# Kernel optimization log

Hardware: AMD Instinct MI355X
Metric: run time of the kernel (lower is better)

## Reference

```python
import jax, jax.numpy as jnp
import numpy as np

B, N, FH, H, FO = 8, 1024, 128, 8, 64
FIN = 2 * FH  # f_hid * 2
NEG = -1e9
SLOPE = 0.2  # leaky_relu negative slope (GAT default)


def setup_inputs() -> dict:
    key = jax.random.key(0)
    ks = jax.random.split(key, 10)
    x = jax.random.normal(ks[0], (B, FIN), jnp.float32)
    A = jax.random.randint(ks[1], (B, N, N), 0, 2, jnp.int32)  # 0/1 dense adjacency
    mask_zero = jnp.ones((B, N, 1), jnp.float32)  # node validity mask
    p_atten = jax.random.uniform(ks[2], (B, N), jnp.float32)  # unused in forward body
    e_atten = jax.random.uniform(ks[3], (B, N, FIN), jnp.float32)
    Npost = jax.random.normal(ks[4], (N, FIN), jnp.float32) * np.float32(1.0 / np.sqrt(FIN))  # kaiming-ish
    w = jax.random.normal(ks[5], (H, FIN, FO), jnp.float32) * np.float32(1.0 / np.sqrt(FIN))
    a_src = jax.random.normal(ks[6], (H, FO), jnp.float32) * np.float32(0.1)
    a_dst = jax.random.normal(ks[7], (H, FO), jnp.float32) * np.float32(0.1)
    bias = jnp.zeros((FO,), jnp.float32)
    return {"x": x, "A": A, "mask_zero": mask_zero, "p_atten": p_atten,
            "e_atten": e_atten, "Npost": Npost, "w": w, "a_src": a_src,
            "a_dst": a_dst, "bias": bias}


def reference(x, A, mask_zero, p_atten, e_atten, Npost, w, a_src, a_dst, bias):
    # broadcast-mul feature gating: x [B,FIN] repeated over N posts, gated by Npost*e_atten
    recx = x[:, None, :] * (Npost[None, :, :] * e_atten)          # [B,N,FIN]
    # BatchGAT (DeepInf-style multi-head graph attention, dropout disabled / eval mode)
    h = jnp.einsum('bnf,hfo->bhno', recx, w)                      # [B,H,N,FO]
    s = jnp.einsum('bhno,ho->bhn', h, a_src)                      # src attention term
    d = jnp.einsum('bhno,ho->bhn', h, a_dst)                      # dst attention term
    logits = jax.nn.leaky_relu(s[:, :, :, None] + d[:, :, None, :], SLOPE)  # [B,H,N,N]
    adj = (A > 0)[:, None, :, :]                                  # [B,1,N,N]
    logits = jnp.where(adj, logits, NEG)
    attn = jax.nn.softmax(logits, axis=-1)                        # masked row softmax
    out = jnp.einsum('bhnm,bhmo->bhno', attn, h) + bias           # aggregate neighbors
    out = out.mean(axis=1)                                        # average heads -> [B,N,FO]
    return out * mask_zero                                        # zero padded nodes
```

## Files before the change

kernel.cpp:

```cpp
#include <hip/hip_runtime.h>

typedef __attribute__((ext_vector_type(8))) short          bf16x8;
typedef __attribute__((ext_vector_type(8))) unsigned short u16x8;
typedef __attribute__((ext_vector_type(4))) unsigned short u16x4;
typedef __attribute__((ext_vector_type(4))) float          f32x4;
typedef __attribute__((ext_vector_type(4))) unsigned int   u32x4;

union U8 { u16x8 u; bf16x8 b; u32x4 w; };
union U4 { u16x4 u; unsigned w[2]; };

__device__ __forceinline__ unsigned short f2bf(float f){
  unsigned u = __float_as_uint(f);
  return (unsigned short)((u + 0x7fffu + ((u >> 16) & 1u)) >> 16);
}
__device__ __forceinline__ unsigned pack_bf16(float lo, float hi){
  unsigned a = __float_as_uint(hi) + 0x8000u;
  unsigned b = __float_as_uint(lo) + 0x8000u;
  return __builtin_amdgcn_perm(a, b, 0x07060302u);
}

#define NN  1024
#define FIN 256
#define NH  8
#define FO  64

__global__ __launch_bounds__(256) void stage0(
    const float* __restrict__ w, const int* __restrict__ A,
    const float* __restrict__ bias, const float* __restrict__ mz,
    unsigned short* __restrict__ wfrag, unsigned long long* __restrict__ Abits,
    float* __restrict__ out)
{
  const int tid = blockIdx.x * 256 + threadIdx.x;
  if (tid < 16384){
    const int lane = tid & 63, ss = (tid >> 6) & 3, kc = (tid >> 8) & 7, h = tid >> 11;
    const int o = 16 * ss + (lane & 15);
    const int f = kc * 32 + (lane >> 4) * 8;
    u16x8 r;
    #pragma unroll
    for (int j = 0; j < 8; j++) r[j] = f2bf(w[(h * FIN + f + j) * FO + o]);
    *(u16x8*)(wfrag + tid * 8) = r;
  }
  #pragma unroll
  for (int k = 0; k < 2; k++){
    const int i = tid + k * 262144;
    out[i] = bias[i & 63] * mz[i >> 6];
  }
  for (int i = tid; i < 8388608; i += 262144){
    unsigned long long m = __ballot(A[i] > 0);
    if ((threadIdx.x & 63) == 0) Abits[i >> 6] = m;
  }
}

__global__ __launch_bounds__(512, 4) void stageA(
    const float* __restrict__ x, const float* __restrict__ e_at,
    const float* __restrict__ Np, const unsigned short* __restrict__ wfrag,
    const float* __restrict__ a_src, const float* __restrict__ a_dst,
    unsigned short* __restrict__ hT,
    float* __restrict__ exps, float* __restrict__ exps2,
    float* __restrict__ expd, float* __restrict__ expd2)
{
  __shared__ unsigned short rex[16 * 264];
  const int t = threadIdx.x;
  const int n0 = blockIdx.x * 16, b = blockIdx.y;

  {
    const int row = t >> 5, f0 = (t & 31) * 8;
    const int nrow = n0 + row;
    const float* ep = e_at + (b * NN + nrow) * FIN + f0;
    const float* qp = Np + nrow * FIN + f0;
    const float* xp = x + b * FIN + f0;
    f32x4 e0 = *(const f32x4*)ep, e1 = *(const f32x4*)(ep + 4);
    f32x4 q0 = *(const f32x4*)qp, q1 = *(const f32x4*)(qp + 4);
    f32x4 x0 = *(const f32x4*)xp, x1 = *(const f32x4*)(xp + 4);
    u16x8 r;
    #pragma unroll
    for (int j = 0; j < 4; j++){
      r[j]     = f2bf(e0[j] * q0[j] * x0[j]);
      r[j + 4] = f2bf(e1[j] * q1[j] * x1[j]);
    }
    *(u16x8*)(rex + row * 264 + f0) = r;
  }
  __syncthreads();

  const int h = t >> 6, lane = t & 63, quad = lane >> 4, l15 = lane & 15;
  const unsigned short* wf = wfrag + h * 16384 + lane * 8;

  f32x4 acc[4] = {};
  #pragma unroll
  for (int kc = 0; kc < 8; kc++){
    U8 a0, bf[4];
    a0.u = *(const u16x8*)(rex + l15 * 264 + kc * 32 + quad * 8);
    #pragma unroll
    for (int ss = 0; ss < 4; ss++) bf[ss].u = *(const u16x8*)(wf + (kc * 4 + ss) * 512);
    #pragma unroll
    for (int ss = 0; ss < 4; ss++)
      acc[ss] = __builtin_amdgcn_mfma_f32_16x16x32_bf16(a0.b, bf[ss].b, acc[ss], 0, 0, 0);
  }

  {
    const int mtile = blockIdx.x >> 1, moff = (blockIdx.x & 1) * 16;
    unsigned short* pan = hT + (size_t)(((b * NH + h) * 32 + mtile) * 64) * 32;
    #pragma unroll
    for (int ss = 0; ss < 4; ss++){
      U4 v;
      v.w[0] = pack_bf16(acc[ss][0], acc[ss][1]);
      v.w[1] = pack_bf16(acc[ss][2], acc[ss][3]);
      *(u16x4*)(pan + (16 * ss + l15) * 32 + moff + quad * 4) = v.u;
    }
  }

  float as4[4], ad4[4];
  #pragma unroll
  for (int ss = 0; ss < 4; ss++){
    as4[ss] = a_src[h * FO + 16 * ss + l15];
    ad4[ss] = a_dst[h * FO + 16 * ss + l15];
  }
  #pragma unroll
  for (int i = 0; i < 4; i++){
    float ps = 0.f, pd = 0.f;
    #pragma unroll
    for (int ss = 0; ss < 4; ss++){ ps += acc[ss][i] * as4[ss]; pd += acc[ss][i] * ad4[ss]; }
    #pragma unroll
    for (int off = 1; off < 16; off <<= 1){
      ps += __shfl_xor(ps, off);
      pd += __shfl_xor(pd, off);
    }
    if (l15 == 0){
      const int idx = (b * NH + h) * NN + n0 + quad * 4 + i;
      exps [idx] = __expf(ps);
      exps2[idx] = __expf(0.2f * ps);
      expd [idx] = __expf(pd);
      expd2[idx] = __expf(0.2f * pd);
    }
  }
}

__global__ __launch_bounds__(512, 8) void stageB(
    const unsigned* __restrict__ Aw,
    const unsigned short* __restrict__ hT,
    const float* __restrict__ exps, const float* __restrict__ exps2,
    const float* __restrict__ expd, const float* __restrict__ expd2,
    const float* __restrict__ mz, float* __restrict__ out)
{
  __shared__ float ed_l[2 * NN];
  __shared__ float e2_l[2 * NN];
  __shared__ unsigned mask_l[32 * 33];
  __shared__ float l_l[4 * 16];
  const int t = threadIdx.x;
  const int n0 = blockIdx.x * 32, hq = blockIdx.y, b = blockIdx.z;
  const int w = t >> 6, lane = t & 63, quad = lane >> 4, l15 = lane & 15;
  const int hl = w & 1, rg = (w >> 1) & 1, mh = w >> 2;
  const int h = hq * 2 + hl;

  if (t < 64) l_l[t] = 0.f;
  {
    const float* s1 = expd  + (b * NH + hq * 2) * NN;
    const float* s2 = expd2 + (b * NH + hq * 2) * NN;
    *(f32x4*)(ed_l + t * 4) = *(const f32x4*)(s1 + t * 4);
    *(f32x4*)(e2_l + t * 4) = *(const f32x4*)(s2 + t * 4);
  }
  #pragma unroll
  for (int k = 0; k < 2; k++){
    const int i = t + k * 512;
    mask_l[(i >> 5) * 33 + (i & 31)] = Aw[(b * NN + n0 + (i >> 5)) * 32 + (i & 31)];
  }
  __syncthreads();

  const int hb = (b * NH + h) * NN;
  const float Es  = exps [hb + n0 + rg * 16 + l15];
  const float Es2 = exps2[hb + n0 + rg * 16 + l15];
  const unsigned short* pb = hT + (size_t)(b * NH + h) * 65536 + l15 * 32 + quad * 8;
  const float* edh = ed_l + hl * NN + quad * 8;
  const float* e2h = e2_l + hl * NN + quad * 8;
  const unsigned* maskp = mask_l + (rg * 16 + l15) * 33;
  const int c0 = mh * 16;

  U8 pan[4];
  #pragma unroll
  for (int ss = 0; ss < 4; ss++)
    pan[ss].u = *(const u16x8*)(pb + (size_t)c0 * 2048 + ss * 512);

  f32x4 acc[4] = {};
  float lp = 0.f;

  for (int cc = 0; cc < 16; cc++){
    const int c = c0 + cc;
    const unsigned am = maskp[c] >> (quad * 8);
    float pv[8];
    #pragma unroll
    for (int g2 = 0; g2 < 2; g2++){
      f32x4 dv = *(const f32x4*)(edh + c * 32 + g2 * 4);
      f32x4 gv = *(const f32x4*)(e2h + c * 32 + g2 * 4);
      #pragma unroll
      for (int j = 0; j < 4; j++){
        float e = fmaxf(Es * dv[j], Es2 * gv[j]);
        pv[g2 * 4 + j] = (am & (1u << (g2 * 4 + j))) ? e : 0.f;
      }
    }
    lp += ((pv[0] + pv[1]) + (pv[2] + pv[3])) + ((pv[4] + pv[5]) + (pv[6] + pv[7]));
    U8 p;
    #pragma unroll
    for (int r = 0; r < 4; r++) p.w[r] = pack_bf16(pv[2 * r], pv[2 * r + 1]);
    #pragma unroll
    for (int ss = 0; ss < 4; ss++)
      acc[ss] = __builtin_amdgcn_mfma_f32_16x16x32_bf16(p.b, pan[ss].b, acc[ss], 0, 0, 0);
    if (cc + 1 < 16){
      #pragma unroll
      for (int ss = 0; ss < 4; ss++)
        pan[ss].u = *(const u16x8*)(pb + (size_t)(c + 1) * 2048 + ss * 512);
    }
  }

  lp += __shfl_xor(lp, 16);
  lp += __shfl_xor(lp, 32);
  if (lane < 16) atomicAdd(&l_l[(w & 3) * 16 + lane], lp);
  __syncthreads();

  const float* mzp = mz + b * NN + n0 + rg * 16;
  #pragma unroll
  for (int i = 0; i < 4; i++){
    const int row = quad * 4 + i;
    const float invm = (0.125f / l_l[(w & 3) * 16 + row]) * mzp[row];
    float* op = out + (size_t)(b * NN + n0 + rg * 16 + row) * FO + l15;
    #pragma unroll
    for (int ss = 0; ss < 4; ss++)
      atomicAdd(op + ss * 16, acc[ss][i] * invm);
  }
}

extern "C" void kernel_launch(void* const* d_in, const int* in_sizes, int n_in,
                              void* d_out, int out_size, void* d_ws, size_t ws_size,
                              hipStream_t stream)
{
  (void)in_sizes; (void)n_in; (void)out_size; (void)ws_size;
  const float* x    = (const float*)d_in[0];
  const int*   A    = (const int*)d_in[1];
  const float* mz   = (const float*)d_in[2];
  const float* e_at = (const float*)d_in[4];
  const float* Np   = (const float*)d_in[5];
  const float* w    = (const float*)d_in[6];
  const float* asrc = (const float*)d_in[7];
  const float* adst = (const float*)d_in[8];
  const float* bias = (const float*)d_in[9];
  float* out = (float*)d_out;

  char* ws = (char*)d_ws;
  unsigned short* wfrag = (unsigned short*)ws;
  unsigned short* hT    = (unsigned short*)(ws + 262144);
  float* exps  = (float*)(ws + 8650752);
  float* exps2 = (float*)(ws + 8912896);
  float* expd  = (float*)(ws + 9175040);
  float* expd2 = (float*)(ws + 9437184);
  unsigned long long* Abits = (unsigned long long*)(ws + 9699328);

  stage0<<<dim3(1024), dim3(256), 0, stream>>>(w, A, bias, mz, wfrag, Abits, out);
  stageA<<<dim3(64, 8), dim3(512), 0, stream>>>(x, e_at, Np, wfrag, asrc, adst,
                                                hT, exps, exps2, expd, expd2);
  stageB<<<dim3(32, 4, 8), dim3(512), 0, stream>>>((const unsigned*)Abits, hT,
                                                   exps, exps2, expd, expd2,
                                                   mz, out);
}
```

Measured before the change: 170.4 us.

## Split attention into row-sum pass and column-tiled aggregation with prescaled weights

Replaces the single stageB kernel with two kernels. phaseL computes each row's masked softmax denominator up front and folds 1/sum, the head-averaging factor and the node mask into per-row scale factors. phaseM then tiles over neighbor columns, stages the matching h panel in shared memory once per block and reuses it across all 1024 rows. Each tile's contribution goes to the output through atomics, with no per-block row-sum reduction. This trades an extra launch and computing the exponentials twice for much less re-reading of hT and more independent MFMA work, at the cost of more global atomics.

```diff
diff --git a/kernel.cpp b/kernel.cpp
--- a/kernel.cpp
+++ b/kernel.cpp
@@ -4,6 +4,7 @@
 typedef __attribute__((ext_vector_type(8))) unsigned short u16x8;
 typedef __attribute__((ext_vector_type(4))) unsigned short u16x4;
 typedef __attribute__((ext_vector_type(4))) float          f32x4;
+typedef __attribute__((ext_vector_type(4))) int            i32x4;
 typedef __attribute__((ext_vector_type(4))) unsigned int   u32x4;
 
 union U8 { u16x8 u; bf16x8 b; u32x4 w; };
@@ -135,96 +136,135 @@
   }
 }
 
-__global__ __launch_bounds__(512, 8) void stageB(
+__global__ __launch_bounds__(256, 4) void phaseL(
+    const unsigned* __restrict__ Aw,
+    const float* __restrict__ exps, const float* __restrict__ exps2,
+    const float* __restrict__ expd, const float* __restrict__ expd2,
+    const float* __restrict__ mz, float2* __restrict__ esc)
+{
+  __shared__ float ed[1024], e2[1024];
+  const int t = threadIdx.x;
+  const int h = blockIdx.y, b = blockIdx.z, bh = b * NH + h;
+  *(f32x4*)(ed + t * 4) = *(const f32x4*)(expd  + bh * NN + t * 4);
+  *(f32x4*)(e2 + t * 4) = *(const f32x4*)(expd2 + bh * NN + t * 4);
+  __syncthreads();
+
+  const int row = blockIdx.x * 64 + (t >> 2), q = t & 3;
+  const float Es = exps[bh * NN + row], Es2 = exps2[bh * NN + row];
+  const unsigned* mw = Aw + (b * NN + row) * 32 + q * 8;
+  i32x4 w0 = *(const i32x4*)mw, w1 = *(const i32x4*)(mw + 4);
+
+  float sum = 0.f;
+  #pragma unroll
+  for (int k = 0; k < 8; k++){
+    const unsigned wd = (unsigned)((k < 4) ? w0[k] : w1[k - 4]);
+    const int base = q * 256 + k * 32;
+    #pragma unroll
+    for (int g = 0; g < 8; g++){
+      f32x4 dv = *(const f32x4*)(ed + base + g * 4);
+      f32x4 gv = *(const f32x4*)(e2 + base + g * 4);
+      #pragma unroll
+      for (int j = 0; j < 4; j++){
+        const float e = fmaxf(Es * dv[j], Es2 * gv[j]);
+        sum += (wd & (1u << (g * 4 + j))) ? e : 0.f;
+      }
+    }
+  }
+  sum += __shfl_xor(sum, 1);
+  sum += __shfl_xor(sum, 2);
+  if (q == 0){
+    const float s = 0.125f * mz[b * NN + row] / sum;
+    float2 r; r.x = Es * s; r.y = Es2 * s;
+    esc[bh * NN + row] = r;
+  }
+}
+
+__global__ __launch_bounds__(512, 4) void phaseM(
     const unsigned* __restrict__ Aw,
     const unsigned short* __restrict__ hT,
-    const float* __restrict__ exps, const float* __restrict__ exps2,
     const float* __restrict__ expd, const float* __restrict__ expd2,
-    const float* __restrict__ mz, float* __restrict__ out)
-{
-  __shared__ float ed_l[2 * NN];
-  __shared__ float e2_l[2 * NN];
-  __shared__ unsigned mask_l[32 * 33];
-  __shared__ float l_l[4 * 16];
+    const float2* __restrict__ esc, float* __restrict__ out)
+{
+  __shared__ unsigned short pan[4 * 64 * 40];
+  __shared__ float ed[128], e2[128];
   const int t = threadIdx.x;
-  const int n0 = blockIdx.x * 32, hq = blockIdx.y, b = blockIdx.z;
-  const int w = t >> 6, lane = t & 63, quad = lane >> 4, l15 = lane & 15;
-  const int hl = w & 1, rg = (w >> 1) & 1, mh = w >> 2;
-  const int h = hq * 2 + hl;
-
-  if (t < 64) l_l[t] = 0.f;
+  const int mo = blockIdx.x, h = blockIdx.y, b = blockIdx.z, bh = b * NH + h;
+
   {
-    const float* s1 = expd  + (b * NH + hq * 2) * NN;
-    const float* s2 = expd2 + (b * NH + hq * 2) * NN;
-    *(f32x4*)(ed_l + t * 4) = *(const f32x4*)(s1 + t * 4);
-    *(f32x4*)(e2_l + t * 4) = *(const f32x4*)(s2 + t * 4);
-  }
-  #pragma unroll
-  for (int k = 0; k < 2; k++){
-    const int i = t + k * 512;
-    mask_l[(i >> 5) * 33 + (i & 31)] = Aw[(b * NN + n0 + (i >> 5)) * 32 + (i & 31)];
-  }
+    const unsigned short* src = hT + (size_t)(bh * 32 + mo * 4) * 2048 + t * 16;
+    u16x8 v0 = *(const u16x8*)src;
+    u16x8 v1 = *(const u16x8*)(src + 8);
+    const int g = t * 16, c = g >> 11, rem = g & 2047, o = rem >> 5, m0 = rem & 31;
+    unsigned short* dst = pan + (c * 64 + o) * 40 + m0;
+    *(u16x8*)dst = v0;
+    *(u16x8*)(dst + 8) = v1;
+  }
+  if (t < 32)      *(f32x4*)(ed + t * 4)        = *(const f32x4*)(expd  + bh * NN + mo * 128 + t * 4);
+  else if (t < 64) *(f32x4*)(e2 + (t - 32) * 4) = *(const f32x4*)(expd2 + bh * NN + mo * 128 + (t - 32) * 4);
   __syncthreads();
 
-  const int hb = (b * NH + h) * NN;
-  const float Es  = exps [hb + n0 + rg * 16 + l15];
-  const float Es2 = exps2[hb + n0 + rg * 16 + l15];
-  const unsigned short* pb = hT + (size_t)(b * NH + h) * 65536 + l15 * 32 + quad * 8;
-  const float* edh = ed_l + hl * NN + quad * 8;
-  const float* e2h = e2_l + hl * NN + quad * 8;
-  const unsigned* maskp = mask_l + (rg * 16 + l15) * 33;
-  const int c0 = mh * 16;
-
-  U8 pan[4];
-  #pragma unroll
-  for (int ss = 0; ss < 4; ss++)
-    pan[ss].u = *(const u16x8*)(pb + (size_t)c0 * 2048 + ss * 512);
-
-  f32x4 acc[4] = {};
-  float lp = 0.f;
-
-  for (int cc = 0; cc < 16; cc++){
-    const int c = c0 + cc;
-    const unsigned am = maskp[c] >> (quad * 8);
-    float pv[8];
-    #pragma unroll
-    for (int g2 = 0; g2 < 2; g2++){
-      f32x4 dv = *(const f32x4*)(edh + c * 32 + g2 * 4);
-      f32x4 gv = *(const f32x4*)(e2h + c * 32 + g2 * 4);
+  const int wv = t >> 6, lane = t & 63, quad = lane >> 4, l15 = lane & 15;
+  const unsigned* Ab = Aw + (size_t)(b * NN) * 32 + mo * 4;
+  const float2* ep = esc + bh * NN;
+
+  i32x4 pm0 = *(const i32x4*)(Ab + (size_t)(wv * 32 + l15) * 32);
+  i32x4 pm1 = *(const i32x4*)(Ab + (size_t)(wv * 32 + 16 + l15) * 32);
+  float2 pe0 = ep[wv * 32 + l15];
+  float2 pe1 = ep[wv * 32 + 16 + l15];
+
+  for (int nt = wv; nt < 32; nt += 8){
+    const i32x4 cm0 = pm0, cm1 = pm1;
+    const float2 ce0 = pe0, ce1 = pe1;
+    if (nt + 8 < 32){
+      pm0 = *(const i32x4*)(Ab + (size_t)((nt + 8) * 32 + l15) * 32);
+      pm1 = *(const i32x4*)(Ab + (size_t)((nt + 8) * 32 + 16 + l15) * 32);
+      pe0 = ep[(nt + 8) * 32 + l15];
+      pe1 = ep[(nt + 8) * 32 + 16 + l15];
+    }
+    f32x4 acc[2][4] = {};
+    #pragma unroll
+    for (int c = 0; c < 4; c++){
+      f32x4 dv0 = *(const f32x4*)(ed + c * 32 + quad * 8);
+      f32x4 dv1 = *(const f32x4*)(ed + c * 32 + quad * 8 + 4);
+      f32x4 gv0 = *(const f32x4*)(e2 + c * 32 + quad * 8);
+      f32x4 gv1 = *(const f32x4*)(e2 + c * 32 + quad * 8 + 4);
+      const unsigned a0 = ((unsigned)cm0[c]) >> (quad * 8);
+      const unsigned a1 = ((unsigned)cm1[c]) >> (quad * 8);
+      U8 p0, p1;
       #pragma unroll
-      for (int j = 0; j < 4; j++){
-        float e = fmaxf(Es * dv[j], Es2 * gv[j]);
-        pv[g2 * 4 + j] = (am & (1u << (g2 * 4 + j))) ? e : 0.f;
+      for (int r = 0; r < 4; r++){
+        const int j0 = 2 * r, j1 = 2 * r + 1;
+        const float d0 = (j0 < 4) ? dv0[j0] : dv1[j0 - 4];
+        const float g0 = (j0 < 4) ? gv0[j0] : gv1[j0 - 4];
+        const float d1 = (j1 < 4) ? dv0[j1] : dv1[j1 - 4];
+        const float g1 = (j1 < 4) ? gv0[j1] : gv1[j1 - 4];
+        float e00 = fmaxf(ce0.x * d0, ce0.y * g0);
+        float e01 = fmaxf(ce0.x * d1, ce0.y * g1);
+        float e10 = fmaxf(ce1.x * d0, ce1.y * g0);
+        float e11 = fmaxf(ce1.x * d1, ce1.y * g1);
+        e00 = (a0 & (1u << j0)) ? e00 : 0.f;
+        e01 = (a0 & (1u << j1)) ? e01 : 0.f;
+        e10 = (a1 & (1u << j0)) ? e10 : 0.f;
+        e11 = (a1 & (1u << j1)) ? e11 : 0.f;
+        p0.w[r] = pack_bf16(e00, e01);
+        p1.w[r] = pack_bf16(e10, e11);
       }
-    }
-    lp += ((pv[0] + pv[1]) + (pv[2] + pv[3])) + ((pv[4] + pv[5]) + (pv[6] + pv[7]));
-    U8 p;
-    #pragma unroll
-    for (int r = 0; r < 4; r++) p.w[r] = pack_bf16(pv[2 * r], pv[2 * r + 1]);
-    #pragma unroll
-    for (int ss = 0; ss < 4; ss++)
-      acc[ss] = __builtin_amdgcn_mfma_f32_16x16x32_bf16(p.b, pan[ss].b, acc[ss], 0, 0, 0);
-    if (cc + 1 < 16){
+      #pragma unroll
+      for (int ss = 0; ss < 4; ss++){
+        U8 pf;
+        pf.u = *(const u16x8*)(pan + (c * 64 + 16 * ss + l15) * 40 + quad * 8);
+        acc[0][ss] = __builtin_amdgcn_mfma_f32_16x16x32_bf16(p0.b, pf.b, acc[0][ss], 0, 0, 0);
+        acc[1][ss] = __builtin_amdgcn_mfma_f32_16x16x32_bf16(p1.b, pf.b, acc[1][ss], 0, 0, 0);
+      }
+    }
+    float* ob = out + (size_t)(b * NN + nt * 32) * FO;
+    #pragma unroll
+    for (int rg = 0; rg < 2; rg++)
       #pragma unroll
       for (int ss = 0; ss < 4; ss++)
-        pan[ss].u = *(const u16x8*)(pb + (size_t)(c + 1) * 2048 + ss * 512);
-    }
-  }
-
-  lp += __shfl_xor(lp, 16);
-  lp += __shfl_xor(lp, 32);
-  if (lane < 16) atomicAdd(&l_l[(w & 3) * 16 + lane], lp);
-  __syncthreads();
-
-  const float* mzp = mz + b * NN + n0 + rg * 16;
-  #pragma unroll
-  for (int i = 0; i < 4; i++){
-    const int row = quad * 4 + i;
-    const float invm = (0.125f / l_l[(w & 3) * 16 + row]) * mzp[row];
-    float* op = out + (size_t)(b * NN + n0 + rg * 16 + row) * FO + l15;
-    #pragma unroll
-    for (int ss = 0; ss < 4; ss++)
-      atomicAdd(op + ss * 16, acc[ss][i] * invm);
+        #pragma unroll
+        for (int i = 0; i < 4; i++)
+          atomicAdd(ob + (rg * 16 + quad * 4 + i) * FO + ss * 16 + l15, acc[rg][ss][i]);
   }
 }
 
@@ -252,11 +292,13 @@
   float* expd  = (float*)(ws + 9175040);
   float* expd2 = (float*)(ws + 9437184);
   unsigned long long* Abits = (unsigned long long*)(ws + 9699328);
+  float2* esc = (float2*)(ws + 10747904);
 
   stage0<<<dim3(1024), dim3(256), 0, stream>>>(w, A, bias, mz, wfrag, Abits, out);
   stageA<<<dim3(64, 8), dim3(512), 0, stream>>>(x, e_at, Np, wfrag, asrc, adst,
                                                 hT, exps, exps2, expd, expd2);
-  stageB<<<dim3(32, 4, 8), dim3(512), 0, stream>>>((const unsigned*)Abits, hT,
-                                                   exps, exps2, expd, expd2,
-                                                   mz, out);
-}
+  phaseL<<<dim3(16, 8, 8), dim3(256), 0, stream>>>((const unsigned*)Abits,
+                                                   exps, exps2, expd, expd2, mz, esc);
+  phaseM<<<dim3(8, 8, 8), dim3(512), 0, stream>>>((const unsigned*)Abits, hT,
+                                                  expd, expd2, esc, out);
+}
```

New measurement: 289.4 us. 1.7x slower.

## Retile attention aggregation to one head per block with 64 rows and split neighbors

Applied to the files above, without the earlier changes.

The aggregation kernel now gives each block one head and 64 query rows. The 8 waves split the 32 neighbor chunks between them, four chunks each, and every wave covers all four 16-row groups, so each loaded hT panel is reused across 64 rows instead of 16. Partial outputs from the waves are first reduced in shared memory with LDS atomics, then written to global memory with one atomic per element. The aim is to cut global hT traffic and the number of global atomics. In exchange each wave holds a larger register accumulator, the block uses more LDS, and occupancy drops to 4 blocks per SM.

```diff
diff --git a/kernel.cpp b/kernel.cpp
--- a/kernel.cpp
+++ b/kernel.cpp
@@ -4,6 +4,7 @@
 typedef __attribute__((ext_vector_type(8))) unsigned short u16x8;
 typedef __attribute__((ext_vector_type(4))) unsigned short u16x4;
 typedef __attribute__((ext_vector_type(4))) float          f32x4;
+typedef __attribute__((ext_vector_type(4))) int            i32x4;
 typedef __attribute__((ext_vector_type(4))) unsigned int   u32x4;
 
 union U8 { u16x8 u; bf16x8 b; u32x4 w; };
@@ -135,96 +136,119 @@
   }
 }
 
-__global__ __launch_bounds__(512, 8) void stageB(
+__global__ __launch_bounds__(512, 4) void phaseB(
     const unsigned* __restrict__ Aw,
     const unsigned short* __restrict__ hT,
     const float* __restrict__ exps, const float* __restrict__ exps2,
     const float* __restrict__ expd, const float* __restrict__ expd2,
     const float* __restrict__ mz, float* __restrict__ out)
 {
-  __shared__ float ed_l[2 * NN];
-  __shared__ float e2_l[2 * NN];
-  __shared__ unsigned mask_l[32 * 33];
-  __shared__ float l_l[4 * 16];
+  __shared__ float ed_l[NN];
+  __shared__ float e2_l[NN];
+  __shared__ unsigned mask_l[64 * 33];
+  __shared__ float es_l[64], es2_l[64], sc_l[64], l_l[64];
+  __shared__ float oacc[64 * 65];
   const int t = threadIdx.x;
-  const int n0 = blockIdx.x * 32, hq = blockIdx.y, b = blockIdx.z;
-  const int w = t >> 6, lane = t & 63, quad = lane >> 4, l15 = lane & 15;
-  const int hl = w & 1, rg = (w >> 1) & 1, mh = w >> 2;
-  const int h = hq * 2 + hl;
-
-  if (t < 64) l_l[t] = 0.f;
-  {
-    const float* s1 = expd  + (b * NH + hq * 2) * NN;
-    const float* s2 = expd2 + (b * NH + hq * 2) * NN;
-    *(f32x4*)(ed_l + t * 4) = *(const f32x4*)(s1 + t * 4);
-    *(f32x4*)(e2_l + t * 4) = *(const f32x4*)(s2 + t * 4);
-  }
-  #pragma unroll
-  for (int k = 0; k < 2; k++){
+  const int n0 = blockIdx.x * 64, h = blockIdx.y, b = blockIdx.z;
+  const int bh = b * NH + h;
+
+  if (t < 256) *(f32x4*)(ed_l + t * 4)         = *(const f32x4*)(expd  + bh * NN + t * 4);
+  else         *(f32x4*)(e2_l + (t - 256) * 4) = *(const f32x4*)(expd2 + bh * NN + (t - 256) * 4);
+  #pragma unroll
+  for (int k = 0; k < 4; k++){
     const int i = t + k * 512;
     mask_l[(i >> 5) * 33 + (i & 31)] = Aw[(b * NN + n0 + (i >> 5)) * 32 + (i & 31)];
   }
-  __syncthreads();
-
-  const int hb = (b * NH + h) * NN;
-  const float Es  = exps [hb + n0 + rg * 16 + l15];
-  const float Es2 = exps2[hb + n0 + rg * 16 + l15];
-  const unsigned short* pb = hT + (size_t)(b * NH + h) * 65536 + l15 * 32 + quad * 8;
-  const float* edh = ed_l + hl * NN + quad * 8;
-  const float* e2h = e2_l + hl * NN + quad * 8;
-  const unsigned* maskp = mask_l + (rg * 16 + l15) * 33;
-  const int c0 = mh * 16;
-
-  U8 pan[4];
+  if (t < 64)       es_l [t]       = exps [bh * NN + n0 + t];
+  else if (t < 128) es2_l[t - 64]  = exps2[bh * NN + n0 + t - 64];
+  else if (t < 192) sc_l [t - 128] = mz[b * NN + n0 + t - 128];
+  else if (t < 256) l_l  [t - 192] = 0.f;
+  for (int i = t; i < 64 * 65; i += 512) oacc[i] = 0.f;
+  __syncthreads();
+
+  const int wv = t >> 6, lane = t & 63, quad = lane >> 4, l15 = lane & 15;
+  const unsigned short* pb = hT + (size_t)bh * 65536 + l15 * 32 + quad * 8;
+  const int c0 = wv * 4;
+
+  float Es[4], Es2[4];
+  #pragma unroll
+  for (int rg = 0; rg < 4; rg++){
+    Es[rg]  = es_l [rg * 16 + l15];
+    Es2[rg] = es2_l[rg * 16 + l15];
+  }
+
+  U8 pan[2][4];
   #pragma unroll
   for (int ss = 0; ss < 4; ss++)
-    pan[ss].u = *(const u16x8*)(pb + (size_t)c0 * 2048 + ss * 512);
-
-  f32x4 acc[4] = {};
-  float lp = 0.f;
-
-  for (int cc = 0; cc < 16; cc++){
+    pan[0][ss].u = *(const u16x8*)(pb + (size_t)c0 * 2048 + ss * 512);
+
+  f32x4 acc[4][4] = {};
+  float lp[4] = {0.f, 0.f, 0.f, 0.f};
+
+  #pragma unroll
+  for (int cc = 0; cc < 4; cc++){
     const int c = c0 + cc;
-    const unsigned am = maskp[c] >> (quad * 8);
-    float pv[8];
-    #pragma unroll
-    for (int g2 = 0; g2 < 2; g2++){
-      f32x4 dv = *(const f32x4*)(edh + c * 32 + g2 * 4);
-      f32x4 gv = *(const f32x4*)(e2h + c * 32 + g2 * 4);
-      #pragma unroll
-      for (int j = 0; j < 4; j++){
-        float e = fmaxf(Es * dv[j], Es2 * gv[j]);
-        pv[g2 * 4 + j] = (am & (1u << (g2 * 4 + j))) ? e : 0.f;
+    if (cc + 1 < 4){
+      #pragma unroll
+      for (int ss = 0; ss < 4; ss++)
+        pan[(cc + 1) & 1][ss].u = *(const u16x8*)(pb + (size_t)(c + 1) * 2048 + ss * 512);
+    }
+    f32x4 dv0 = *(const f32x4*)(ed_l + c * 32 + quad * 8);
+    f32x4 dv1 = *(const f32x4*)(ed_l + c * 32 + quad * 8 + 4);
+    f32x4 gv0 = *(const f32x4*)(e2_l + c * 32 + quad * 8);
+    f32x4 gv1 = *(const f32x4*)(e2_l + c * 32 + quad * 8 + 4);
+    #pragma unroll
+    for (int rg = 0; rg < 4; rg++){
+      const unsigned ab = mask_l[(rg * 16 + l15) * 33 + c] >> (quad * 8);
+      float pv[8];
+      #pragma unroll
+      for (int j = 0; j < 8; j++){
+        const float d = (j < 4) ? dv0[j] : dv1[j - 4];
+        const float g = (j < 4) ? gv0[j] : gv1[j - 4];
+        const float e = fmaxf(Es[rg] * d, Es2[rg] * g);
+        pv[j] = (ab & (1u << j)) ? e : 0.f;
       }
-    }
-    lp += ((pv[0] + pv[1]) + (pv[2] + pv[3])) + ((pv[4] + pv[5]) + (pv[6] + pv[7]));
-    U8 p;
-    #pragma unroll
-    for (int r = 0; r < 4; r++) p.w[r] = pack_bf16(pv[2 * r], pv[2 * r + 1]);
+      lp[rg] += ((pv[0] + pv[1]) + (pv[2] + pv[3])) + ((pv[4] + pv[5]) + (pv[6] + pv[7]));
+      U8 p;
+      #pragma unroll
+      for (int r = 0; r < 4; r++) p.w[r] = pack_bf16(pv[2 * r], pv[2 * r + 1]);
+      #pragma unroll
+      for (int ss = 0; ss < 4; ss++)
+        acc[rg][ss] = __builtin_amdgcn_mfma_f32_16x16x32_bf16(p.b, pan[cc & 1][ss].b, acc[rg][ss], 0, 0, 0);
+    }
+  }
+
+  #pragma unroll
+  for (int rg = 0; rg < 4; rg++){
+    lp[rg] += __shfl_xor(lp[rg], 16);
+    lp[rg] += __shfl_xor(lp[rg], 32);
+  }
+  if (lane < 16){
+    #pragma unroll
+    for (int rg = 0; rg < 4; rg++)
+      atomicAdd(&l_l[rg * 16 + lane], lp[rg]);
+  }
+  __syncthreads();
+
+  #pragma unroll
+  for (int rg = 0; rg < 4; rg++){
+    float s[4];
+    #pragma unroll
+    for (int i = 0; i < 4; i++){
+      const int row = rg * 16 + quad * 4 + i;
+      s[i] = 0.125f * sc_l[row] / l_l[row];
+    }
     #pragma unroll
     for (int ss = 0; ss < 4; ss++)
-      acc[ss] = __builtin_amdgcn_mfma_f32_16x16x32_bf16(p.b, pan[ss].b, acc[ss], 0, 0, 0);
-    if (cc + 1 < 16){
-      #pragma unroll
-      for (int ss = 0; ss < 4; ss++)
-        pan[ss].u = *(const u16x8*)(pb + (size_t)(c + 1) * 2048 + ss * 512);
-    }
-  }
-
-  lp += __shfl_xor(lp, 16);
-  lp += __shfl_xor(lp, 32);
-  if (lane < 16) atomicAdd(&l_l[(w & 3) * 16 + lane], lp);
-  __syncthreads();
-
-  const float* mzp = mz + b * NN + n0 + rg * 16;
-  #pragma unroll
-  for (int i = 0; i < 4; i++){
-    const int row = quad * 4 + i;
-    const float invm = (0.125f / l_l[(w & 3) * 16 + row]) * mzp[row];
-    float* op = out + (size_t)(b * NN + n0 + rg * 16 + row) * FO + l15;
-    #pragma unroll
-    for (int ss = 0; ss < 4; ss++)
-      atomicAdd(op + ss * 16, acc[ss][i] * invm);
+      #pragma unroll
+      for (int i = 0; i < 4; i++)
+        atomicAdd(&oacc[(rg * 16 + quad * 4 + i) * 65 + ss * 16 + l15], acc[rg][ss][i] * s[i]);
+  }
+  __syncthreads();
+
+  for (int i = t; i < 4096; i += 512){
+    const int r = i >> 6, o = i & 63;
+    atomicAdd(out + (size_t)(b * NN + n0 + r) * FO + o, oacc[r * 65 + o]);
   }
 }
 
@@ -256,7 +280,7 @@
   stage0<<<dim3(1024), dim3(256), 0, stream>>>(w, A, bias, mz, wfrag, Abits, out);
   stageA<<<dim3(64, 8), dim3(512), 0, stream>>>(x, e_at, Np, wfrag, asrc, adst,
                                                 hT, exps, exps2, expd, expd2);
-  stageB<<<dim3(32, 4, 8), dim3(512), 0, stream>>>((const unsigned*)Abits, hT,
+  phaseB<<<dim3(16, 8, 8), dim3(512), 0, stream>>>((const unsigned*)Abits, hT,
                                                    exps, exps2, expd, expd2,
                                                    mz, out);
 }
```

Result: slower. 349.9 us (+105.4%).
